# Kernel tuning notes

Hardware: AMD Instinct MI355X
Metric: run time of the kernel (lower is better)

Reference implementation:

```python
import jax, jax.numpy as jnp
import numpy as np

S = 256  # vocab_size == num_states (required for the original code to broadcast)
B = 16
L = 512


def sparsemax(z):
    # sparsemax over the last axis (Martins & Astudillo 2016)
    zs = -jnp.sort(-z, axis=-1)                      # descending sort
    k = jnp.arange(1, z.shape[-1] + 1, dtype=z.dtype)
    zc = jnp.cumsum(zs, axis=-1)
    supp = 1.0 + k * zs > zc                         # support mask
    kz = supp.sum(axis=-1, keepdims=True)
    tau = (jnp.take_along_axis(zc, kz - 1, axis=-1) - 1.0) / kz.astype(z.dtype)
    return jnp.maximum(z - tau, 0.0)


def sparsemax_loss_vec(z):
    # Fenchel-Young sparsemax loss against EVERY class y:
    #   loss[..., y] = <z, p*> - 0.5||p*||^2 + 0.5 - z_y,  p* = sparsemax(z)
    p = sparsemax(z)
    c = (z * p).sum(-1, keepdims=True) - 0.5 * (p * p).sum(-1, keepdims=True) + 0.5
    return c - z


def setup_inputs() -> dict:
    key = jax.random.key(0)
    k1, k2, k3, k4, k5 = jax.random.split(key, 5)
    xs = jax.random.randint(k1, (B, L), 1, S)   # tokens in [1, S); 0 is padding
    alpha = jax.random.normal(k2, (1, S)) * 0.1
    omega = jax.random.normal(k3, (1, S)) * 0.1
    E = jax.random.normal(k4, (S, S)) * 0.1
    T = jax.random.normal(k5, (S, S, S)) * 0.1
    return {"xs": xs, "alpha": alpha, "omega": omega, "E": E, "T": T}


def reference(xs, alpha, omega, E, T):
    S_ = E.shape[0]
    mask = xs != 0                         # padding mask (padding=0)
    # Precompute loss tables (vectorizes all sparsemax_loss calls of the original)
    LE = sparsemax_loss_vec(E)             # (S, S):   LE[q, x]
    LT = sparsemax_loss_vec(T)             # (S, S, S): LT[q, x, next]
    LOm = sparsemax_loss_vec(omega)[0]     # (S,)  chart[:, K]
    LAl = sparsemax_loss_vec(alpha)[0]     # (S,)
    LE_x = LE.T                            # (x, q)
    LT_x = jnp.transpose(LT, (1, 0, 2))    # (x, q, next)

    c0 = jnp.broadcast_to(LOm, (xs.shape[0], S_))  # (B, S) chart at t = K

    def step(c, inp):
        x_t, m_t = inp                     # (B,), (B,)
        # chart[q, t] = LE[q, x_t] + logsumexp(LT[q, x_t, :] + chart[:, t+1])
        new = LE_x[x_t] + jax.nn.logsumexp(LT_x[x_t] + c[:, None, :], axis=-1)
        return jnp.where(m_t[:, None], new, c), None

    # backward recursion t = K-1 .. 0  ->  scan over time-reversed tokens
    c_final, _ = jax.lax.scan(step, c0, (xs[:, ::-1].T, mask[:, ::-1].T))

    per_seq = jax.nn.logsumexp(LAl[None, :] + c_final, axis=-1)  # (B,)
    return jnp.sum(per_seq)[None]          # matches torch shape (1,)
```

## Files before the change

kernel.cpp:

```cpp
#include <hip/hip_runtime.h>
#include <hip/hip_fp16.h>

#define LDIM 512
#define BDIM 16

#define WS_A    0u
#define WS_CE   262144u
#define WS_LOM  263168u
#define WS_LAL  264192u
#define WS_PS   265216u
#define WS_W    270336u
#define WS_FAST_BYTES (270336ull + 16777216ull)

typedef float f32x4 __attribute__((ext_vector_type(4)));

__device__ __forceinline__ float wred_add(float v) {
    #pragma unroll
    for (int off = 32; off; off >>= 1) v += __shfl_xor(v, off);
    return v;
}
__device__ __forceinline__ float wred_max(float v) {
    #pragma unroll
    for (int off = 32; off; off >>= 1) v = fmaxf(v, __shfl_xor(v, off));
    return v;
}

#if __has_builtin(__builtin_amdgcn_cvt_pk_f32_fp8) && __has_builtin(__builtin_amdgcn_cvt_pk_fp8_f32)
#define HW_FP8 1
#else
#define HW_FP8 0
#endif

__device__ __forceinline__ unsigned int sw_fp8_enc(float a) {
    union { float f; unsigned int u; } x; x.f = a;
    unsigned int u = x.u + 0x80000u;
    return (((u >> 23) & 0xffu) - 120u) * 8u + ((u >> 20) & 7u);
}
__device__ __forceinline__ unsigned int pack4_fp8(float a, float b, float c, float d) {
#if HW_FP8
    int v = 0;
    v = __builtin_amdgcn_cvt_pk_fp8_f32(a, b, v, false);
    v = __builtin_amdgcn_cvt_pk_fp8_f32(c, d, v, true);
    return (unsigned int)v;
#else
    return sw_fp8_enc(a) | (sw_fp8_enc(b) << 8) | (sw_fp8_enc(c) << 16) | (sw_fp8_enc(d) << 24);
#endif
}

__device__ __forceinline__ long mk64(unsigned int lo, unsigned int hi) {
    return (long)(((unsigned long long)hi << 32) | (unsigned long long)lo);
}

__device__ float sparsemax_c4(float z0, float z1, float z2, float z3) {
    float ssum = wred_add(z0 + z1 + z2 + z3);
    float tau = (ssum - 1.0f) * (1.0f / 256.0f);
    int kprev = 256;
    for (int it = 0; it < 64; ++it) {
        float s = 0.f, cnt = 0.f;
        if (z0 > tau) { s += z0; cnt += 1.f; }
        if (z1 > tau) { s += z1; cnt += 1.f; }
        if (z2 > tau) { s += z2; cnt += 1.f; }
        if (z3 > tau) { s += z3; cnt += 1.f; }
        s = wred_add(s);
        cnt = wred_add(cnt);
        tau = (s - 1.0f) / cnt;
        int k = (int)cnt;
        if (k == kprev) break;
        kprev = k;
    }
    float cs = 0.f, t2 = tau * tau;
    if (z0 > tau) cs += z0 * z0 - t2;
    if (z1 > tau) cs += z1 * z1 - t2;
    if (z2 > tau) cs += z2 * z2 - t2;
    if (z3 > tau) cs += z3 * z3 - t2;
    cs = wred_add(cs);
    return 0.5f * cs + 0.5f;
}

__global__ __launch_bounds__(256) void k_erow(const float* E, const float* omega,
                                              const float* alpha,
                                              float* cE, float* LOm, float* LAl) {
    int wid = blockIdx.x * 4 + (threadIdx.x >> 6);
    if (wid >= 258) return;
    int lane = threadIdx.x & 63;
    const float* row = (wid < 256) ? (E + wid * 256)
                      : (wid == 256 ? omega : alpha);
    float4 z = *(const float4*)(row + lane * 4);
    float c = sparsemax_c4(z.x, z.y, z.z, z.w);
    if (wid < 256) {
        if (lane == 0) cE[wid] = c;
    } else {
        float* dst = (wid == 256) ? LOm : LAl;
        *(float4*)(dst + lane * 4) = make_float4(c - z.x, c - z.y, c - z.z, c - z.w);
    }
}

__global__ __launch_bounds__(256) void k_trow(const float* T, unsigned char* W8,
                                              float* A, int writeW) {
    int wid = blockIdx.x * 4 + (threadIdx.x >> 6);
    int lane = threadIdx.x & 63;
    int x = wid >> 8, q = wid & 255;
    const float* row = T + ((size_t)((q << 8) | x) << 8);
    float4 z = *(const float4*)(row + lane * 4);
    float c = sparsemax_c4(z.x, z.y, z.z, z.w);
    if (writeW) {
        unsigned int packed = pack4_fp8(__expf(-z.x), __expf(-z.y),
                                        __expf(-z.z), __expf(-z.w));
        int n0 = lane << 2;
        size_t off = ((size_t)x << 16) + ((size_t)(q >> 4) << 12)
                   + ((size_t)(n0 >> 6) << 10)
                   + ((size_t)((n0 >> 3) & 3) << 8)
                   + ((size_t)(q & 15) << 4)
                   + ((size_t)((n0 >> 5) & 1) << 3)
                   + (size_t)(n0 & 7);
        *(unsigned int*)(W8 + off) = packed;
    }
    if (lane == 0) A[wid] = c;
}

__global__ __launch_bounds__(256) void k_afix(const float* E, const float* cE, float* A) {
    int x = blockIdx.x, q = threadIdx.x;
    int idx = (x << 8) + q;
    A[idx] = __expf(A[idx] + cE[q] - E[q * 256 + x]);
}

#define PF(XV, D0, D1, D2, D3, EAD) do {                                 \
    const unsigned char* p_ = WqBase + ((size_t)(XV) << 16);             \
    D0 = *(const uint4*)(p_);                                            \
    D1 = *(const uint4*)(p_ + 1024);                                     \
    D2 = *(const uint4*)(p_ + 2048);                                     \
    D3 = *(const uint4*)(p_ + 3072);                                     \
    EAD = *(const float4*)(EAg + ((XV) << 8));                           \
} while (0)

#define STEPX(XC, W0, W1_, W2_, W3_, EAV) do {                           \
    if ((XC) != 0) {                                                     \
        float rr_ = rs[pb];                                              \
        const uint4* bv_ = (const uint4*)u8b[pb];                        \
        uint4 B0 = bv_[(g << 2) + 0];                                    \
        uint4 B1 = bv_[(g << 2) + 1];                                    \
        uint4 B2 = bv_[(g << 2) + 2];                                    \
        uint4 B3 = bv_[(g << 2) + 3];                                    \
        f32x4 ac0 = {0.f, 0.f, 0.f, 0.f}, ac1 = {0.f, 0.f, 0.f, 0.f};    \
        ac0 = __builtin_amdgcn_mfma_f32_16x16x32_fp8_fp8(mk64(W0.x, W0.y),  mk64(B0.x, B0.y), ac0, 0, 0, 0); \
        ac1 = __builtin_amdgcn_mfma_f32_16x16x32_fp8_fp8(mk64(W0.z, W0.w),  mk64(B0.z, B0.w), ac1, 0, 0, 0); \
        ac0 = __builtin_amdgcn_mfma_f32_16x16x32_fp8_fp8(mk64(W1_.x, W1_.y), mk64(B1.x, B1.y), ac0, 0, 0, 0); \
        ac1 = __builtin_amdgcn_mfma_f32_16x16x32_fp8_fp8(mk64(W1_.z, W1_.w), mk64(B1.z, B1.w), ac1, 0, 0, 0); \
        ac0 = __builtin_amdgcn_mfma_f32_16x16x32_fp8_fp8(mk64(W2_.x, W2_.y), mk64(B2.x, B2.y), ac0, 0, 0, 0); \
        ac1 = __builtin_amdgcn_mfma_f32_16x16x32_fp8_fp8(mk64(W2_.z, W2_.w), mk64(B2.z, B2.w), ac1, 0, 0, 0); \
        ac0 = __builtin_amdgcn_mfma_f32_16x16x32_fp8_fp8(mk64(W3_.x, W3_.y), mk64(B3.x, B3.y), ac0, 0, 0, 0); \
        ac1 = __builtin_amdgcn_mfma_f32_16x16x32_fp8_fp8(mk64(W3_.z, W3_.w), mk64(B3.z, B3.w), ac1, 0, 0, 0); \
        f32x4 sv = ac0 + ac1;    \
        if (isw) {                                                       \
            float4 nu;                                                   \
            nu.x = EAV.x * sv.x * rr_;                                   \
            nu.y = EAV.y * sv.y * rr_;                                   \
            nu.z = EAV.z * sv.z * rr_;                                   \
            nu.w = EAV.w * sv.w * rr_;                                   \
            u_last = nu;                                                 \
            u8b[pb ^ 1][wdw] = pack4_fp8(nu.x, nu.y, nu.z, nu.w);        \
        }                                                                \
        if (tid == 0) { rs[pb ^ 1] = 0.0625f / fmaxf(sv.x, 1e-30f);      \
                        LM -= __logf(rr_); }                             \
    } else {                                                             \
        if (isw) u8b[pb ^ 1][wdw] = u8b[pb][wdw];     \
        if (tid == 0) rs[pb ^ 1] = rs[pb];                               \
    }                                                                    \
    pb ^= 1;                                                             \
    __syncthreads();                                                     \
} while (0)

__global__ __launch_bounds__(1024) void k_main_fast(const int* xs, const unsigned char* W8,
                                                    const float* EA, const float* LOm,
                                                    const float* LAl, float* per_seq) {
    int b = blockIdx.x, tid = threadIdx.x;
    int lane = tid & 63, w = tid >> 6, g = lane >> 4;
    __shared__ int xsh[LDIM];
    __shared__ float red[4];
    __shared__ float rs[2];
    __shared__ float lm_sh;
    __shared__ __align__(16) unsigned int u8b[2][64];
    __shared__ __align__(16) float u_f[256];
    if (tid < LDIM) xsh[tid] = xs[b * LDIM + tid];
    if (tid < 64) {
        int gg = tid >> 4, c = (tid >> 1) & 7, j0 = (tid & 1) << 2;
        int n0 = (c << 5) + (gg << 3) + j0;
        float4 lv = *(const float4*)(LOm + n0);
        u8b[0][tid] = pack4_fp8(__expf(lv.x), __expf(lv.y), __expf(lv.z), __expf(lv.w));
    }
    if (tid == 0) { rs[0] = 0.0625f / 256.0f; rs[1] = rs[0]; }
    __syncthreads();

    float LM = 0.f;
    int pb = 0;
    int isw = ((lane & 15) == 0);
    int q0 = (w << 4) + (g << 2);
    int wdw = (((q0 >> 3) & 3) << 4) + ((q0 >> 5) << 1) + ((q0 & 7) >> 2);
    float4 u_last = make_float4(1.f, 1.f, 1.f, 1.f);
    const unsigned char* WqBase = W8 + ((size_t)w << 12) + ((size_t)lane << 4);
    const float* EAg = EA + (w << 4) + (g << 2);

    uint4 a0, a1, a2, a3, b0, b1, b2, b3;
    float4 eaA, eaB;
    int xA = xsh[511], xB = xsh[510];
    PF(xA, a0, a1, a2, a3, eaA);
    for (int t = 511; t > 0; t -= 2) {
        PF(xB, b0, b1, b2, b3, eaB);
        int xAn = (t >= 3) ? xsh[t - 2] : 0;
        int xBn = (t >= 3) ? xsh[t - 3] : 0;
        STEPX(xA, a0, a1, a2, a3, eaA);
        PF(xAn, a0, a1, a2, a3, eaA);
        STEPX(xB, b0, b1, b2, b3, eaB);
        xA = xAn; xB = xBn;
    }

    if (isw) *(float4*)(u_f + q0) = u_last;
    if (tid == 0) lm_sh = LM;
    __syncthreads();
    float v = -3.0e38f;
    if (tid < 256) v = LAl[tid] + __logf(fmaxf(u_f[tid], 1e-37f));
    float m2 = wred_max(v);
    if (tid < 256 && (tid & 63) == 0) red[tid >> 6] = m2;
    __syncthreads();
    m2 = fmaxf(fmaxf(red[0], red[1]), fmaxf(red[2], red[3]));
    float e = (tid < 256) ? __expf(v - m2) : 0.f;
    float es = wred_add(e);
    __syncthreads();
    if (tid < 256 && (tid & 63) == 0) red[tid >> 6] = es;
    __syncthreads();
    if (tid == 0) per_seq[b] = lm_sh + m2 + __logf(red[0] + red[1] + red[2] + red[3]);
}

__global__ __launch_bounds__(256) void k_main_med(const int* xs, const float* T,
                                                  const float* A, const float* LOm,
                                                  const float* LAl, float* per_seq) {
    int b = blockIdx.x, q = threadIdx.x;
    __shared__ int xsh[LDIM];
    __shared__ float red[4];
    __shared__ __align__(16) float u_f[256];
    for (int i = q; i < LDIM; i += 256) xsh[i] = xs[b * LDIM + i];
    float c = LOm[q];
    __syncthreads();
    for (int t = LDIM - 1; t >= 0; --t) {
        int x = xsh[t];
        if (x != 0) {
            float m = wred_max(c);
            if ((q & 63) == 0) red[q >> 6] = m;
            __syncthreads();
            m = fmaxf(fmaxf(red[0], red[1]), fmaxf(red[2], red[3]));
            u_f[q] = __expf(c - m);
            __syncthreads();
            const float* Tp = T + (((size_t)(q << 8) + (size_t)x) << 8);
            float acc = 0.f;
            #pragma unroll 4
            for (int i = 0; i < 32; ++i) {
                float4 ta = *(const float4*)(Tp + (i << 3));
                float4 tb = *(const float4*)(Tp + (i << 3) + 4);
                float4 ua = *(const float4*)(u_f + (i << 3));
                float4 ub = *(const float4*)(u_f + (i << 3) + 4);
                acc = fmaf(__expf(-ta.x), ua.x, acc);
                acc = fmaf(__expf(-ta.y), ua.y, acc);
                acc = fmaf(__expf(-ta.z), ua.z, acc);
                acc = fmaf(__expf(-ta.w), ua.w, acc);
                acc = fmaf(__expf(-tb.x), ub.x, acc);
                acc = fmaf(__expf(-tb.y), ub.y, acc);
                acc = fmaf(__expf(-tb.z), ub.z, acc);
                acc = fmaf(__expf(-tb.w), ub.w, acc);
            }
            acc = fmaxf(acc, 1e-30f);
            c = __logf(A[(x << 8) + q]) + m + __logf(acc);
        }
    }
    float v = LAl[q] + c;
    float m2 = wred_max(v);
    if ((q & 63) == 0) red[q >> 6] = m2;
    __syncthreads();
    m2 = fmaxf(fmaxf(red[0], red[1]), fmaxf(red[2], red[3]));
    float es = wred_add(__expf(v - m2));
    __syncthreads();
    if ((q & 63) == 0) red[q >> 6] = es;
    __syncthreads();
    if (q == 0) per_seq[b] = m2 + __logf(red[0] + red[1] + red[2] + red[3]);
}

__global__ __launch_bounds__(64) void k_final(const float* per_seq, float* out) {
    if (threadIdx.x == 0) {
        float s = 0.f;
        for (int i = 0; i < BDIM; ++i) s += per_seq[i];
        out[0] = s;
    }
}

extern "C" void kernel_launch(void* const* d_in, const int* in_sizes, int n_in,
                              void* d_out, int out_size, void* d_ws, size_t ws_size,
                              hipStream_t stream) {
    const int* xs = nullptr;
    const float *alpha = nullptr, *omega = nullptr, *E = nullptr, *T = nullptr;
    int seen256 = 0;
    for (int i = 0; i < n_in; ++i) {
        int s = in_sizes[i];
        if      (s == 16777216) T  = (const float*)d_in[i];
        else if (s == 65536)    E  = (const float*)d_in[i];
        else if (s == 8192)     xs = (const int*)d_in[i];
        else if (s == 256) { if (seen256++ == 0) alpha = (const float*)d_in[i];
                             else                omega = (const float*)d_in[i]; }
    }

    char* ws = (char*)d_ws;
    float* EA       = (float*)(ws + WS_A);
    float* cE       = (float*)(ws + WS_CE);
    float* LOm      = (float*)(ws + WS_LOM);
    float* LAl      = (float*)(ws + WS_LAL);
    float* per_seq  = (float*)(ws + WS_PS);
    unsigned char* W8 = (unsigned char*)(ws + WS_W);
    int fast = (ws_size >= WS_FAST_BYTES) ? 1 : 0;

    k_erow<<<65, 256, 0, stream>>>(E, omega, alpha, cE, LOm, LAl);
    k_trow<<<16384, 256, 0, stream>>>(T, W8, EA, fast);
    k_afix<<<256, 256, 0, stream>>>(E, cE, EA);
    if (fast) k_main_fast<<<BDIM, 1024, 0, stream>>>(xs, W8, EA, LOm, LAl, per_seq);
    else      k_main_med <<<BDIM, 256, 0, stream>>>(xs, T, EA, LOm, LAl, per_seq);
    k_final<<<1, 64, 0, stream>>>(per_seq, (float*)d_out);
}
```

Measured before the change: 538.4 us.

## Fuse EA fixup into trow, deepen scan prefetch, spread fp8 writes across lanes

Folds the k_afix exp correction into k_trow, removing one kernel launch and one pass over the EA table. The main scan now keeps four timesteps of weights in flight instead of two, to hide more global-load latency in the serial recursion. Each of four lanes per group writes one fp8 byte rather than one lane packing four, which shortens the per-step critical path. The __syncthreads is replaced by a raw lgkmcnt wait plus s_barrier, which relies on LDS-only ordering between steps and raises register pressure from the extra prefetch buffers.

```diff
diff --git a/kernel.cpp b/kernel.cpp
--- a/kernel.cpp
+++ b/kernel.cpp
@@ -46,9 +46,24 @@
     return sw_fp8_enc(a) | (sw_fp8_enc(b) << 8) | (sw_fp8_enc(c) << 16) | (sw_fp8_enc(d) << 24);
 #endif
 }
+__device__ __forceinline__ unsigned char fp8_1(float a) {
+#if HW_FP8
+    return (unsigned char)(__builtin_amdgcn_cvt_pk_fp8_f32(a, a, 0, false) & 0xff);
+#else
+    return (unsigned char)sw_fp8_enc(a);
+#endif
+}
 
 __device__ __forceinline__ long mk64(unsigned int lo, unsigned int hi) {
     return (long)(((unsigned long long)hi << 32) | (unsigned long long)lo);
+}
+
+__device__ __forceinline__ void sync_lds() {
+    asm volatile("s_waitcnt lgkmcnt(0)" ::: "memory");
+    __builtin_amdgcn_sched_barrier(0);
+    __builtin_amdgcn_s_barrier();
+    __builtin_amdgcn_sched_barrier(0);
+    asm volatile("" ::: "memory");
 }
 
 __device__ float sparsemax_c4(float z0, float z1, float z2, float z3) {
@@ -95,8 +110,9 @@
     }
 }
 
-__global__ __launch_bounds__(256) void k_trow(const float* T, unsigned char* W8,
-                                              float* A, int writeW) {
+__global__ __launch_bounds__(256) void k_trow(const float* T, const float* E,
+                                              const float* cE, unsigned char* W8,
+                                              float* EA, int writeW) {
     int wid = blockIdx.x * 4 + (threadIdx.x >> 6);
     int lane = threadIdx.x & 63;
     int x = wid >> 8, q = wid & 255;
@@ -115,35 +131,29 @@
                    + (size_t)(n0 & 7);
         *(unsigned int*)(W8 + off) = packed;
     }
-    if (lane == 0) A[wid] = c;
-}
-
-__global__ __launch_bounds__(256) void k_afix(const float* E, const float* cE, float* A) {
-    int x = blockIdx.x, q = threadIdx.x;
-    int idx = (x << 8) + q;
-    A[idx] = __expf(A[idx] + cE[q] - E[q * 256 + x]);
-}
-
-#define PF(XV, D0, D1, D2, D3, EAD) do {                                 \
+    if (lane == 0) EA[wid] = __expf(c + cE[q] - E[(q << 8) + x]);
+}
+
+#define PF(XV, D0, D1, D2, D3, EAS) do {                                 \
     const unsigned char* p_ = WqBase + ((size_t)(XV) << 16);             \
     D0 = *(const uint4*)(p_);                                            \
     D1 = *(const uint4*)(p_ + 1024);                                     \
     D2 = *(const uint4*)(p_ + 2048);                                     \
     D3 = *(const uint4*)(p_ + 3072);                                     \
-    EAD = *(const float4*)(EAg + ((XV) << 8));                           \
+    EAS = EAq[(XV) << 8];                                                \
 } while (0)
 
-#define STEPX(XC, W0, W1_, W2_, W3_, EAV) do {                           \
+#define STEPX(XC, W0, W1_, W2_, W3_, EAS) do {                           \
+    float rr_ = rs2[pb];                                                 \
     if ((XC) != 0) {                                                     \
-        float rr_ = rs[pb];                                              \
         const uint4* bv_ = (const uint4*)u8b[pb];                        \
         uint4 B0 = bv_[(g << 2) + 0];                                    \
         uint4 B1 = bv_[(g << 2) + 1];                                    \
         uint4 B2 = bv_[(g << 2) + 2];                                    \
         uint4 B3 = bv_[(g << 2) + 3];                                    \
         f32x4 ac0 = {0.f, 0.f, 0.f, 0.f}, ac1 = {0.f, 0.f, 0.f, 0.f};    \
-        ac0 = __builtin_amdgcn_mfma_f32_16x16x32_fp8_fp8(mk64(W0.x, W0.y),  mk64(B0.x, B0.y), ac0, 0, 0, 0); \
-        ac1 = __builtin_amdgcn_mfma_f32_16x16x32_fp8_fp8(mk64(W0.z, W0.w),  mk64(B0.z, B0.w), ac1, 0, 0, 0); \
+        ac0 = __builtin_amdgcn_mfma_f32_16x16x32_fp8_fp8(mk64(W0.x, W0.y),   mk64(B0.x, B0.y), ac0, 0, 0, 0); \
+        ac1 = __builtin_amdgcn_mfma_f32_16x16x32_fp8_fp8(mk64(W0.z, W0.w),   mk64(B0.z, B0.w), ac1, 0, 0, 0); \
         ac0 = __builtin_amdgcn_mfma_f32_16x16x32_fp8_fp8(mk64(W1_.x, W1_.y), mk64(B1.x, B1.y), ac0, 0, 0, 0); \
         ac1 = __builtin_amdgcn_mfma_f32_16x16x32_fp8_fp8(mk64(W1_.z, W1_.w), mk64(B1.z, B1.w), ac1, 0, 0, 0); \
         ac0 = __builtin_amdgcn_mfma_f32_16x16x32_fp8_fp8(mk64(W2_.x, W2_.y), mk64(B2.x, B2.y), ac0, 0, 0, 0); \
@@ -151,23 +161,21 @@
         ac0 = __builtin_amdgcn_mfma_f32_16x16x32_fp8_fp8(mk64(W3_.x, W3_.y), mk64(B3.x, B3.y), ac0, 0, 0, 0); \
         ac1 = __builtin_amdgcn_mfma_f32_16x16x32_fp8_fp8(mk64(W3_.z, W3_.w), mk64(B3.z, B3.w), ac1, 0, 0, 0); \
         f32x4 sv = ac0 + ac1;    \
+        float svr = (r_ == 0) ? sv.x : (r_ == 1) ? sv.y                  \
+                  : (r_ == 2) ? sv.z : sv.w;                             \
         if (isw) {                                                       \
-            float4 nu;                                                   \
-            nu.x = EAV.x * sv.x * rr_;                                   \
-            nu.y = EAV.y * sv.y * rr_;                                   \
-            nu.z = EAV.z * sv.z * rr_;                                   \
-            nu.w = EAV.w * sv.w * rr_;                                   \
-            u_last = nu;                                                 \
-            u8b[pb ^ 1][wdw] = pack4_fp8(nu.x, nu.y, nu.z, nu.w);        \
+            float nu = (EAS) * svr * rr_;                                \
+            u_lastS = nu;                                                \
+            u8c[((pb ^ 1) << 8) + wbyte] = fp8_1(nu);                    \
         }                                                                \
-        if (tid == 0) { rs[pb ^ 1] = 0.0625f / fmaxf(sv.x, 1e-30f);      \
+        if (tid == 0) { rs2[pb ^ 1] = 0.0625f / fmaxf(sv.x, 1e-30f);     \
                         LM -= __logf(rr_); }                             \
     } else {                                                             \
-        if (isw) u8b[pb ^ 1][wdw] = u8b[pb][wdw];     \
-        if (tid == 0) rs[pb ^ 1] = rs[pb];                               \
+        if (isw) u8c[((pb ^ 1) << 8) + wbyte] = u8c[(pb << 8) + wbyte];  \
+        if (tid == 0) rs2[pb ^ 1] = rs2[pb];                             \
     }                                                                    \
     pb ^= 1;                                                             \
-    __syncthreads();                                                     \
+    sync_lds();                                                          \
 } while (0)
 
 __global__ __launch_bounds__(1024) void k_main_fast(const int* xs, const unsigned char* W8,
@@ -175,46 +183,56 @@
                                                     const float* LAl, float* per_seq) {
     int b = blockIdx.x, tid = threadIdx.x;
     int lane = tid & 63, w = tid >> 6, g = lane >> 4;
+    int r_ = lane & 3;
     __shared__ int xsh[LDIM];
     __shared__ float red[4];
-    __shared__ float rs[2];
+    __shared__ float rs2[2];
     __shared__ float lm_sh;
     __shared__ __align__(16) unsigned int u8b[2][64];
     __shared__ __align__(16) float u_f[256];
+    unsigned char* u8c = (unsigned char*)u8b;
     if (tid < LDIM) xsh[tid] = xs[b * LDIM + tid];
     if (tid < 64) {
-        int gg = tid >> 4, c = (tid >> 1) & 7, j0 = (tid & 1) << 2;
-        int n0 = (c << 5) + (gg << 3) + j0;
+        int gg = tid >> 4, cch = (tid >> 1) & 7, j0 = (tid & 1) << 2;
+        int n0 = (cch << 5) + (gg << 3) + j0;
         float4 lv = *(const float4*)(LOm + n0);
         u8b[0][tid] = pack4_fp8(__expf(lv.x), __expf(lv.y), __expf(lv.z), __expf(lv.w));
     }
-    if (tid == 0) { rs[0] = 0.0625f / 256.0f; rs[1] = rs[0]; }
+    if (tid < 2) rs2[tid] = 0.0625f / 256.0f;
     __syncthreads();
 
     float LM = 0.f;
     int pb = 0;
-    int isw = ((lane & 15) == 0);
+    int isw = ((lane & 15) < 4);
     int q0 = (w << 4) + (g << 2);
     int wdw = (((q0 >> 3) & 3) << 4) + ((q0 >> 5) << 1) + ((q0 & 7) >> 2);
-    float4 u_last = make_float4(1.f, 1.f, 1.f, 1.f);
+    int wbyte = (wdw << 2) + r_;
+    float u_lastS = 1.f;
     const unsigned char* WqBase = W8 + ((size_t)w << 12) + ((size_t)lane << 4);
-    const float* EAg = EA + (w << 4) + (g << 2);
-
-    uint4 a0, a1, a2, a3, b0, b1, b2, b3;
-    float4 eaA, eaB;
-    int xA = xsh[511], xB = xsh[510];
-    PF(xA, a0, a1, a2, a3, eaA);
-    for (int t = 511; t > 0; t -= 2) {
-        PF(xB, b0, b1, b2, b3, eaB);
-        int xAn = (t >= 3) ? xsh[t - 2] : 0;
-        int xBn = (t >= 3) ? xsh[t - 3] : 0;
-        STEPX(xA, a0, a1, a2, a3, eaA);
-        PF(xAn, a0, a1, a2, a3, eaA);
-        STEPX(xB, b0, b1, b2, b3, eaB);
-        xA = xAn; xB = xBn;
-    }
-
-    if (isw) *(float4*)(u_f + q0) = u_last;
+    const float* EAq = EA + q0 + r_;
+
+    uint4 A0, A1, A2, A3, Bb0, Bb1, Bb2, Bb3, C0, C1, C2, C3, D0, D1, D2, D3;
+    float eA, eB, eC, eD;
+    int x0 = xsh[511], x1 = xsh[510], x2 = xsh[509], x3 = xsh[508];
+    PF(x0, A0, A1, A2, A3, eA);
+    PF(x1, Bb0, Bb1, Bb2, Bb3, eB);
+    PF(x2, C0, C1, C2, C3, eC);
+    PF(x3, D0, D1, D2, D3, eD);
+    for (int it = 0; it < 128; ++it) {
+        int t = 511 - (it << 2);
+        int pf = t - 4;
+        int y0 = (pf >= 0) ? xsh[pf]     : 0;
+        int y1 = (pf >= 1) ? xsh[pf - 1] : 0;
+        int y2 = (pf >= 2) ? xsh[pf - 2] : 0;
+        int y3 = (pf >= 3) ? xsh[pf - 3] : 0;
+        STEPX(x0, A0, A1, A2, A3, eA);     PF(y0, A0, A1, A2, A3, eA);
+        STEPX(x1, Bb0, Bb1, Bb2, Bb3, eB); PF(y1, Bb0, Bb1, Bb2, Bb3, eB);
+        STEPX(x2, C0, C1, C2, C3, eC);     PF(y2, C0, C1, C2, C3, eC);
+        STEPX(x3, D0, D1, D2, D3, eD);     PF(y3, D0, D1, D2, D3, eD);
+        x0 = y0; x1 = y1; x2 = y2; x3 = y3;
+    }
+
+    if (isw) u_f[q0 + r_] = u_lastS;
     if (tid == 0) lm_sh = LM;
     __syncthreads();
     float v = -3.0e38f;
@@ -316,8 +334,7 @@
     int fast = (ws_size >= WS_FAST_BYTES) ? 1 : 0;
 
     k_erow<<<65, 256, 0, stream>>>(E, omega, alpha, cE, LOm, LAl);
-    k_trow<<<16384, 256, 0, stream>>>(T, W8, EA, fast);
-    k_afix<<<256, 256, 0, stream>>>(E, cE, EA);
+    k_trow<<<16384, 256, 0, stream>>>(T, E, cE, W8, EA, fast);
     if (fast) k_main_fast<<<BDIM, 1024, 0, stream>>>(xs, W8, EA, LOm, LAl, per_seq);
     else      k_main_med <<<BDIM, 256, 0, stream>>>(xs, T, EA, LOm, LAl, per_seq);
     k_final<<<1, 64, 0, stream>>>(per_seq, (float*)d_out);
```

Result: faster. 524.2 us (-2.6%).
